# Optimization experiments

Hardware: AMD Instinct MI355X
Metric: run time of the kernel (lower is better)

## Reference

```python
import jax, jax.numpy as jnp
import numpy as np

D = 9  # nodefeat_n1 = 3 (resnet feat) + 6 (pos)


def _lstm_scan(x, Wih, Whh, bih, bhh, reverse=False):
    # x: [T, B, D] -> hidden states [T, B, D]; torch gate order i,f,g,o
    B = x.shape[1]
    def step(carry, xt):
        h, c = carry
        g = xt @ Wih.T + bih + h @ Whh.T + bhh
        i = jax.nn.sigmoid(g[:, :D])
        f = jax.nn.sigmoid(g[:, D:2*D])
        gg = jnp.tanh(g[:, 2*D:3*D])
        o = jax.nn.sigmoid(g[:, 3*D:])
        c = f * c + i * gg
        h = o * jnp.tanh(c)
        return (h, c), h
    init = (jnp.zeros((B, D), x.dtype), jnp.zeros((B, D), x.dtype))
    _, hs = jax.lax.scan(step, init, x, reverse=reverse)
    return hs


def _forward(nodes_feature, pos, attmat, msg_W, msg_b, gru_Wih, gru_Whh, gru_bih, gru_bhh,
             ro1_W, ro1_b, ro2_W, ro2_b, lf_Wih, lf_Whh, lf_bih, lf_bhh,
             lb_Wih, lb_Whh, lb_bih, lb_bhh, lr1_W, lr1_b, lr2_W, lr2_b, num_rec):
    node_feat = jnp.concatenate([nodes_feature, pos], axis=-1)  # [N,T,M,D]
    N, T, M, _ = node_feat.shape
    # valid_node_num = num_rec[b, 0] in the original code
    valid = (jnp.arange(M)[None, :] < num_rec[:, 0:1]).astype(node_feat.dtype)  # [N,M]
    att = attmat * valid[:, None, None, :]  # zero out invalid source nodes q
    src = node_feat  # message sources (h_w)
    hv = node_feat   # GRU hidden (h_v)
    hidden = node_feat
    for _ in range(2):  # iterN = 2 message-passing rounds
        msg = src @ msg_W.T + msg_b                    # [N,T,M,D] message_fc
        m = jnp.einsum('btnq,btqd->btnd', att, msg)    # attention-weighted sum over q
        # single-step GRU cell (torch gate order r,z,n)
        gx = m @ gru_Wih.T + gru_bih
        gh = hv @ gru_Whh.T + gru_bhh
        r = jax.nn.sigmoid(gx[..., :D] + gh[..., :D])
        z = jax.nn.sigmoid(gx[..., D:2*D] + gh[..., D:2*D])
        n = jnp.tanh(gx[..., 2*D:] + r * gh[..., 2*D:])
        h_new = (1.0 - z) * n + z * hv
        hidden = h_new * valid[:, None, :, None]       # invalid nodes never updated -> stay zero
        src = hidden
        hv = hidden
    vmask = valid[:, None, :, None]
    # per-frame readout (pred_label0)
    p0 = jax.nn.relu(hidden @ ro1_W.T + ro1_b) @ ro2_W.T + ro2_b
    pred_label0 = p0 * vmask
    # bidirectional LSTM over time, batched over (batch, node)
    x = hidden.transpose(1, 0, 2, 3).reshape(T, N * M, D)  # [T, N*M, D]
    hf = _lstm_scan(x, lf_Wih, lf_Whh, lf_bih, lf_bhh, reverse=False)
    hb = _lstm_scan(x, lb_Wih, lb_Whh, lb_bih, lb_bhh, reverse=True)
    out = jnp.concatenate([hf, hb], axis=-1).reshape(T, N, M, 2 * D).transpose(1, 0, 2, 3)
    p = jax.nn.relu(out @ lr1_W.T + lr1_b) @ lr2_W.T + lr2_b
    pred_label = p * vmask
    return pred_label, pred_label0


def setup_inputs() -> dict:
    key = jax.random.key(0)
    ks = jax.random.split(key, 32)
    N, T, M = 8192, 20, 6
    def u(k, shape, fan_in):
        s = 1.0 / np.sqrt(fan_in).astype(np.float32)
        return jax.random.uniform(k, shape, jnp.float32, -s, s)
    return {
        "nodes_feature": jax.random.normal(ks[0], (N, T, M, 3), jnp.float32),
        "pos": jax.random.normal(ks[1], (N, T, M, 6), jnp.float32),
        "attmat": jax.random.uniform(ks[2], (N, T, M, M), jnp.float32),
        "msg_W": u(ks[3], (D, D), D), "msg_b": u(ks[4], (D,), D),
        "gru_Wih": u(ks[5], (3 * D, D), D), "gru_Whh": u(ks[6], (3 * D, D), D),
        "gru_bih": u(ks[7], (3 * D,), D), "gru_bhh": u(ks[8], (3 * D,), D),
        "ro1_W": u(ks[9], (D, D), D), "ro1_b": u(ks[10], (D,), D),
        "ro2_W": u(ks[11], (7, D), D), "ro2_b": u(ks[12], (7,), D),
        "lf_Wih": u(ks[13], (4 * D, D), D), "lf_Whh": u(ks[14], (4 * D, D), D),
        "lf_bih": u(ks[15], (4 * D,), D), "lf_bhh": u(ks[16], (4 * D,), D),
        "lb_Wih": u(ks[17], (4 * D, D), D), "lb_Whh": u(ks[18], (4 * D, D), D),
        "lb_bih": u(ks[19], (4 * D,), D), "lb_bhh": u(ks[20], (4 * D,), D),
        "lr1_W": u(ks[21], (D, 2 * D), 2 * D), "lr1_b": u(ks[22], (D,), 2 * D),
        "lr2_W": u(ks[23], (7, D), D), "lr2_b": u(ks[24], (7,), D),
        "num_rec": jax.random.randint(ks[25], (N, T), 1, M + 1),
    }


def reference(nodes_feature, pos, attmat, msg_W, msg_b, gru_Wih, gru_Whh, gru_bih, gru_bhh,
              ro1_W, ro1_b, ro2_W, ro2_b, lf_Wih, lf_Whh, lf_bih, lf_bhh,
              lb_Wih, lb_Whh, lb_bih, lb_bhh, lr1_W, lr1_b, lr2_W, lr2_b, num_rec):
    return _forward(nodes_feature, pos, attmat, msg_W, msg_b, gru_Wih, gru_Whh, gru_bih, gru_bhh,
                    ro1_W, ro1_b, ro2_W, ro2_b, lf_Wih, lf_Whh, lf_bih, lf_bhh,
                    lb_Wih, lb_Whh, lb_bih, lb_bhh, lr1_W, lr1_b, lr2_W, lr2_b, num_rec)
```

## Files before the change

### kernel.cpp

```cpp
#include <hip/hip_runtime.h>

#define N_    8192
#define T_    20
#define M_    6
#define D_    9
#define NM_   (N_*M_)
#define NT_   (N_*T_)
#define NTM7_ (N_*T_*M_*7)

#define LOG2E 1.44269504088896f

typedef __attribute__((ext_vector_type(2))) float v2f;

__device__ __forceinline__ float sigm(float x){
    return __builtin_amdgcn_rcpf(1.f + __builtin_amdgcn_exp2f(-LOG2E * x));
}
__device__ __forceinline__ float tanh_(float x){
    return fmaf(2.f, __builtin_amdgcn_rcpf(1.f + __builtin_amdgcn_exp2f(-2.f*LOG2E * x)), -1.f);
}
__device__ __forceinline__ v2f splat(float s){ return (v2f){s, s}; }
__device__ __forceinline__ v2f sigm2(v2f x){ v2f r; r.x = sigm(x.x); r.y = sigm(x.y); return r; }
__device__ __forceinline__ v2f tanh2(v2f x){ v2f r; r.x = tanh_(x.x); r.y = tanh_(x.y); return r; }
__device__ __forceinline__ v2f relu2(v2f x){ v2f r; r.x = fmaxf(x.x,0.f); r.y = fmaxf(x.y,0.f); return r; }

__device__ __forceinline__ v2f pkfma(v2f a, v2f b, v2f acc){
    asm("v_pk_fma_f32 %0, %1, %2, %0" : "+v"(acc) : "v"(a), "v"(b));
    return acc;
}
__device__ __forceinline__ v2f pkmul(v2f a, v2f b){
    v2f d;
    asm("v_pk_mul_f32 %0, %1, %2" : "=v"(d) : "v"(a), "v"(b));
    return d;
}

__global__ __launch_bounds__(64) void k_fused(
    const float* __restrict__ nf,
    const float* __restrict__ pos,
    const float* __restrict__ am,
    const float* __restrict__ msgW, const float* __restrict__ msgb,
    const float* __restrict__ gWih, const float* __restrict__ gWhh,
    const float* __restrict__ gbih, const float* __restrict__ gbhh,
    const float* __restrict__ ro1W, const float* __restrict__ ro1b,
    const float* __restrict__ ro2W, const float* __restrict__ ro2b,
    const float* __restrict__ fWih, const float* __restrict__ fWhh,
    const float* __restrict__ fbih, const float* __restrict__ fbhh,
    const float* __restrict__ bWih, const float* __restrict__ bWhh,
    const float* __restrict__ bbih, const float* __restrict__ bbhh,
    const float* __restrict__ lr1W, const float* __restrict__ lr1b,
    const float* __restrict__ lr2W, const float* __restrict__ lr2b,
    const int*   __restrict__ numrec,
    float* __restrict__ out,
    float* __restrict__ out0)
{
    __shared__ float  hx[T_ * 3 * D_ * 2];
    __shared__ float4 hxs4[7 * 11];
    __shared__ v2f    shpool[640];

    const int lane = threadIdx.x & 63;
    const int n    = blockIdx.x;

    {
        const int g    = lane / 6;
        const int i    = lane - g * 6;
        const int gB   = g * 58;
        const bool lactive = (lane < 60);

        const int wbase = n * 20;
        const int ntA = lactive ? (wbase + g)      : wbase;
        const int ntB = lactive ? (wbase + 10 + g) : wbase;
        const int nA = ntA / T_, tA = ntA - nA * T_;
        const int nB = ntB / T_, tB = ntB - nB * T_;

        v2f s[D_];
        {
            const float* pA = nf + (size_t)ntA * 18 + i * 3;
            const float* pB = nf + (size_t)ntB * 18 + i * 3;
            #pragma unroll
            for (int k = 0; k < 3; ++k) { s[k].x = pA[k]; s[k].y = pB[k]; }
        }
        {
            const float2* pA = (const float2*)(pos + (size_t)ntA * 36 + i * 6);
            const float2* pB = (const float2*)(pos + (size_t)ntB * 36 + i * 6);
            #pragma unroll
            for (int k = 0; k < 3; ++k) {
                float2 a = pA[k], b = pB[k];
                s[3 + 2*k]     = (v2f){a.x, b.x};
                s[3 + 2*k + 1] = (v2f){a.y, b.y};
            }
        }
        v2f attr[M_];
        {
            const float2* pA = (const float2*)(am + (size_t)ntA * 36 + i * 6);
            const float2* pB = (const float2*)(am + (size_t)ntB * 36 + i * 6);
            #pragma unroll
            for (int k = 0; k < 3; ++k) {
                float2 a = pA[k], b = pB[k];
                attr[2*k]     = (v2f){a.x, b.x};
                attr[2*k + 1] = (v2f){a.y, b.y};
            }
        }
        const int nrA = numrec[nA * T_];
        const int nrB = numrec[nB * T_];
        #pragma unroll
        for (int q = 0; q < M_; ++q) {
            attr[q].x *= (q < nrA) ? 1.f : 0.f;
            attr[q].y *= (q < nrB) ? 1.f : 0.f;
        }
        v2f vmi; vmi.x = (i < nrA) ? 1.f : 0.f; vmi.y = (i < nrB) ? 1.f : 0.f;

        #pragma unroll
        for (int it = 0; it < 2; ++it) {
            #pragma unroll
            for (int d = 0; d < D_; ++d) {
                v2f a = splat(msgb[d]);
                #pragma unroll
                for (int k = 0; k < D_; ++k) a += s[k] * msgW[d*9 + k];
                shpool[gB + d*6 + i] = a;
            }
            v2f mm[D_];
            #pragma unroll
            for (int d = 0; d < D_; ++d) {
                const float4* rp = (const float4*)&shpool[gB + d*6];
                float4 p0 = rp[0], p1 = rp[1], p2 = rp[2];
                v2f a = pkmul(attr[0], (v2f){p0.x, p0.y});
                a = pkfma(attr[1], (v2f){p0.z, p0.w}, a);
                a = pkfma(attr[2], (v2f){p1.x, p1.y}, a);
                a = pkfma(attr[3], (v2f){p1.z, p1.w}, a);
                a = pkfma(attr[4], (v2f){p2.x, p2.y}, a);
                a = pkfma(attr[5], (v2f){p2.z, p2.w}, a);
                mm[d] = a;
            }
            v2f grz[18], gxn[9], ghn[9];
            #pragma unroll
            for (int j = 0; j < 18; ++j) {
                v2f a = splat(gbih[j] + gbhh[j]);
                #pragma unroll
                for (int k = 0; k < D_; ++k) {
                    a += mm[k] * gWih[j*9 + k];
                    a += s[k]  * gWhh[j*9 + k];
                }
                grz[j] = a;
            }
            #pragma unroll
            for (int j = 0; j < 9; ++j) {
                v2f ax = splat(gbih[18 + j]), ah = splat(gbhh[18 + j]);
                #pragma unroll
                for (int k = 0; k < D_; ++k) {
                    ax += mm[k] * gWih[(18 + j)*9 + k];
                    ah += s[k]  * gWhh[(18 + j)*9 + k];
                }
                gxn[j] = ax; ghn[j] = ah;
            }
            #pragma unroll
            for (int d = 0; d < D_; ++d) {
                v2f r  = sigm2(grz[d]);
                v2f z  = sigm2(grz[9 + d]);
                v2f nn = tanh2(gxn[d] + r * ghn[d]);
                s[d] = vmi * ((splat(1.f) - z) * nn + z * s[d]);
            }
        }

        if (lactive) {
            const int pr = i >> 1, par = i & 1;
            #pragma unroll
            for (int d = 0; d < D_; ++d) {
                hx[((tA*3 + pr)*9 + d)*2 + par] = s[d].x;
                hx[((tB*3 + pr)*9 + d)*2 + par] = s[d].y;
            }
        }

        v2f q9[D_];
        #pragma unroll
        for (int d = 0; d < D_; ++d) {
            v2f a = splat(ro1b[d]);
            #pragma unroll
            for (int k = 0; k < D_; ++k) a += s[k] * ro1W[d*9 + k];
            q9[d] = relu2(a);
        }
        if (lactive) {
            float* opA = out0 + (size_t)ntA * 42 + i * 7;
            float* opB = out0 + (size_t)ntB * 42 + i * 7;
            #pragma unroll
            for (int j = 0; j < 7; ++j) {
                v2f a = splat(ro2b[j]);
                #pragma unroll
                for (int k = 0; k < D_; ++k) a += q9[k] * ro2W[j*9 + k];
                a *= vmi;
                opA[j] = a.x; opB[j] = a.y;
            }
        }
    }

    __syncthreads();

    {
        int grpL = lane / 9;
        if (grpL == 7) grpL = 6;
        const int dd  = (lane == 63) ? 0 : (lane - grpL * 9);
        const bool sv   = (grpL < 6);
        const int  p    = sv ? (grpL % 3) : 0;
        const int  dir  = sv ? (grpL / 3) : 0;
        const int  xrow = grpL * 11;

        const float* Wih = dir ? bWih : fWih;
        const float* Whh = dir ? bWhh : fWhh;
        const float* Bih = dir ? bbih : fbih;
        const float* Bhh = dir ? bbhh : fbhh;

        float wxi[9], wxf[9], wxg[9], wxo[9];
        v2f   whi[9], whf[9], whg[9], who[9], w1r[9];
        #pragma unroll
        for (int k = 0; k < 9; ++k) {
            wxi[k] = Wih[(dd     )*9 + k];  whi[k] = splat(Whh[(dd     )*9 + k]);
            wxf[k] = Wih[(9  + dd)*9 + k];  whf[k] = splat(Whh[(9  + dd)*9 + k]);
            wxg[k] = Wih[(18 + dd)*9 + k];  whg[k] = splat(Whh[(18 + dd)*9 + k]);
            wxo[k] = Wih[(27 + dd)*9 + k];  who[k] = splat(Whh[(27 + dd)*9 + k]);
            w1r[k] = splat(lr1W[dd*18 + dir*9 + k]);
        }
        const float bi = Bih[dd]      + Bhh[dd];
        const float bf = Bih[9 + dd]  + Bhh[9 + dd];
        const float bg = Bih[18 + dd] + Bhh[18 + dd];
        const float bo = Bih[27 + dd] + Bhh[27 + dd];

        const int t0 = dir ? (T_ - 1) : 0;
        const int ts = dir ? -1 : 1;

        {
            v2f x0 = *(const v2f*)&hx[((t0*3 + p)*9 + dd)*2];
            hxs4[xrow + dd] = make_float4(0.f, 0.f, x0.x, x0.y);
        }
        v2f h = splat(0.f), c = splat(0.f);
        #pragma unroll 1
        for (int ss = 0; ss < T_; ++ss) {
            const int t = t0 + ts * ss;
            v2f xn = splat(0.f);
            if (ss < T_ - 1) xn = *(const v2f*)&hx[(((t + ts)*3 + p)*9 + dd)*2];

            v2f gi = splat(bi), gf = splat(bf), gg = splat(bg), go = splat(bo);
            v2f qc = splat(0.f);
            #pragma unroll
            for (int j = 0; j < 9; ++j) {
                float4 v = hxs4[xrow + j];
                v2f hj = (v2f){v.x, v.y}, xj = (v2f){v.z, v.w};
                gi = pkfma(hj, whi[j], gi);  gi += xj * wxi[j];
                gf = pkfma(hj, whf[j], gf);  gf += xj * wxf[j];
                gg = pkfma(hj, whg[j], gg);  gg += xj * wxg[j];
                go = pkfma(hj, who[j], go);  go += xj * wxo[j];
                qc = pkfma(hj, w1r[j], qc);
            }

            if (ss > 0 && sv) {
                const int tq = dir ? (20 - ss) : (ss - 1);
                const int qa = (p*20 + tq)*10 + dd;
                if (ss <= 10) shpool[qa] = qc;
                else          shpool[qa] += qc;
            }

            c = sigm2(gf) * c + sigm2(gi) * tanh2(gg);
            h = sigm2(go) * tanh2(c);
            hxs4[xrow + dd] = make_float4(h.x, h.y, xn.x, xn.y);
        }

        {
            v2f qc = splat(0.f);
            #pragma unroll
            for (int j = 0; j < 9; ++j) {
                float4 v = hxs4[xrow + j];
                qc = pkfma((v2f){v.x, v.y}, w1r[j], qc);
            }
            if (sv) {
                const int tq = dir ? 0 : 19;
                shpool[(p*20 + tq)*10 + dd] += qc;
            }
        }
    }

    __syncthreads();

    if (lane < 60) {
        const int pp = lane / 20;
        const int t  = lane - pp * 20;
        const v2f* qrow = &shpool[(pp*20 + t)*10];

        v2f q[9];
        #pragma unroll
        for (int dd2 = 0; dd2 < 9; ++dd2)
            q[dd2] = relu2(qrow[dd2] + splat(lr1b[dd2]));

        const int mA2 = 2 * pp, mB2 = mA2 + 1;
        const int nr = numrec[n * T_];
        v2f vi;
        vi.x = (mA2 < nr) ? 1.f : 0.f;
        vi.y = (mB2 < nr) ? 1.f : 0.f;

        float* opA = out + (size_t)((n * T_ + t) * M_ + mA2) * 7;
        float* opB = out + (size_t)((n * T_ + t) * M_ + mB2) * 7;
        #pragma unroll
        for (int j = 0; j < 7; ++j) {
            v2f a = splat(lr2b[j]);
            #pragma unroll
            for (int k = 0; k < 9; ++k) a += q[k] * lr2W[j*9 + k];
            a *= vi;
            opA[j] = a.x; opB[j] = a.y;
        }
    }
}

extern "C" void kernel_launch(void* const* d_in, const int* in_sizes, int n_in,
                              void* d_out, int out_size, void* d_ws, size_t ws_size,
                              hipStream_t stream) {
    const float* nf    = (const float*)d_in[0];
    const float* pos   = (const float*)d_in[1];
    const float* am    = (const float*)d_in[2];
    const float* msgW  = (const float*)d_in[3];
    const float* msgb  = (const float*)d_in[4];
    const float* gWih  = (const float*)d_in[5];
    const float* gWhh  = (const float*)d_in[6];
    const float* gbih  = (const float*)d_in[7];
    const float* gbhh  = (const float*)d_in[8];
    const float* ro1W  = (const float*)d_in[9];
    const float* ro1b  = (const float*)d_in[10];
    const float* ro2W  = (const float*)d_in[11];
    const float* ro2b  = (const float*)d_in[12];
    const float* lfWih = (const float*)d_in[13];
    const float* lfWhh = (const float*)d_in[14];
    const float* lfbih = (const float*)d_in[15];
    const float* lfbhh = (const float*)d_in[16];
    const float* lbWih = (const float*)d_in[17];
    const float* lbWhh = (const float*)d_in[18];
    const float* lbbih = (const float*)d_in[19];
    const float* lbbhh = (const float*)d_in[20];
    const float* lr1W  = (const float*)d_in[21];
    const float* lr1b  = (const float*)d_in[22];
    const float* lr2W  = (const float*)d_in[23];
    const float* lr2b  = (const float*)d_in[24];
    const int* numrec  = (const int*)d_in[25];

    float* outp = (float*)d_out;
    float* out0 = (float*)d_out + NTM7_;

    k_fused<<<N_, 64, 0, stream>>>(nf, pos, am, msgW, msgb, gWih, gWhh,
                                   gbih, gbhh, ro1W, ro1b, ro2W, ro2b,
                                   lfWih, lfWhh, lfbih, lfbhh,
                                   lbWih, lbWhh, lbbih, lbbhh,
                                   lr1W, lr1b, lr2W, lr2b, numrec,
                                   outp, out0);
}
```

Measured before the change: 266.4 us.

## Process two batch elements per block, interleaving their LSTM recurrences

```diff
diff --git a/kernel.cpp b/kernel.cpp
--- a/kernel.cpp
+++ b/kernel.cpp
@@ -52,14 +52,16 @@
     float* __restrict__ out,
     float* __restrict__ out0)
 {
-    __shared__ float  hx[T_ * 3 * D_ * 2];
-    __shared__ float4 hxs4[7 * 11];
-    __shared__ v2f    shpool[640];
+    __shared__ float  hx[2][T_ * 3 * D_ * 2];
+    __shared__ float4 hxs4[2][7 * 11];
+    __shared__ v2f    shpool[2][640];
 
     const int lane = threadIdx.x & 63;
-    const int n    = blockIdx.x;
-
-    {
+    const int n0   = blockIdx.x * 2;
+
+    #pragma unroll 1
+    for (int nn = 0; nn < 2; ++nn) {
+        const int n    = n0 + nn;
         const int g    = lane / 6;
         const int i    = lane - g * 6;
         const int gB   = g * 58;
@@ -115,12 +117,12 @@
                 v2f a = splat(msgb[d]);
                 #pragma unroll
                 for (int k = 0; k < D_; ++k) a += s[k] * msgW[d*9 + k];
-                shpool[gB + d*6 + i] = a;
+                shpool[nn][gB + d*6 + i] = a;
             }
             v2f mm[D_];
             #pragma unroll
             for (int d = 0; d < D_; ++d) {
-                const float4* rp = (const float4*)&shpool[gB + d*6];
+                const float4* rp = (const float4*)&shpool[nn][gB + d*6];
                 float4 p0 = rp[0], p1 = rp[1], p2 = rp[2];
                 v2f a = pkmul(attr[0], (v2f){p0.x, p0.y});
                 a = pkfma(attr[1], (v2f){p0.z, p0.w}, a);
@@ -155,8 +157,8 @@
             for (int d = 0; d < D_; ++d) {
                 v2f r  = sigm2(grz[d]);
                 v2f z  = sigm2(grz[9 + d]);
-                v2f nn = tanh2(gxn[d] + r * ghn[d]);
-                s[d] = vmi * ((splat(1.f) - z) * nn + z * s[d]);
+                v2f nn2 = tanh2(gxn[d] + r * ghn[d]);
+                s[d] = vmi * ((splat(1.f) - z) * nn2 + z * s[d]);
             }
         }
 
@@ -164,8 +166,8 @@
             const int pr = i >> 1, par = i & 1;
             #pragma unroll
             for (int d = 0; d < D_; ++d) {
-                hx[((tA*3 + pr)*9 + d)*2 + par] = s[d].x;
-                hx[((tB*3 + pr)*9 + d)*2 + par] = s[d].y;
+                hx[nn][((tA*3 + pr)*9 + d)*2 + par] = s[d].x;
+                hx[nn][((tB*3 + pr)*9 + d)*2 + par] = s[d].y;
             }
         }
 
@@ -224,84 +226,116 @@
 
         const int t0 = dir ? (T_ - 1) : 0;
         const int ts = dir ? -1 : 1;
-
-        {
-            v2f x0 = *(const v2f*)&hx[((t0*3 + p)*9 + dd)*2];
-            hxs4[xrow + dd] = make_float4(0.f, 0.f, x0.x, x0.y);
-        }
-        v2f h = splat(0.f), c = splat(0.f);
+        const int xoff = ((t0*3 + p)*9 + dd)*2;
+
+        {
+            v2f x0 = *(const v2f*)&hx[0][xoff];
+            hxs4[0][xrow + dd] = make_float4(0.f, 0.f, x0.x, x0.y);
+            v2f x1 = *(const v2f*)&hx[1][xoff];
+            hxs4[1][xrow + dd] = make_float4(0.f, 0.f, x1.x, x1.y);
+        }
+        v2f h0 = splat(0.f), c0 = splat(0.f);
+        v2f h1 = splat(0.f), c1 = splat(0.f);
+
         #pragma unroll 1
         for (int ss = 0; ss < T_; ++ss) {
             const int t = t0 + ts * ss;
-            v2f xn = splat(0.f);
-            if (ss < T_ - 1) xn = *(const v2f*)&hx[(((t + ts)*3 + p)*9 + dd)*2];
-
-            v2f gi = splat(bi), gf = splat(bf), gg = splat(bg), go = splat(bo);
-            v2f qc = splat(0.f);
+            v2f xn0 = splat(0.f), xn1 = splat(0.f);
+            if (ss < T_ - 1) {
+                const int xo = (((t + ts)*3 + p)*9 + dd)*2;
+                xn0 = *(const v2f*)&hx[0][xo];
+                xn1 = *(const v2f*)&hx[1][xo];
+            }
+
+            v2f gi0 = splat(bi), gf0 = splat(bf), gg0 = splat(bg), go0 = splat(bo);
+            v2f qc0 = splat(0.f);
             #pragma unroll
             for (int j = 0; j < 9; ++j) {
-                float4 v = hxs4[xrow + j];
+                float4 v = hxs4[0][xrow + j];
                 v2f hj = (v2f){v.x, v.y}, xj = (v2f){v.z, v.w};
-                gi = pkfma(hj, whi[j], gi);  gi += xj * wxi[j];
-                gf = pkfma(hj, whf[j], gf);  gf += xj * wxf[j];
-                gg = pkfma(hj, whg[j], gg);  gg += xj * wxg[j];
-                go = pkfma(hj, who[j], go);  go += xj * wxo[j];
-                qc = pkfma(hj, w1r[j], qc);
+                gi0 = pkfma(hj, whi[j], gi0);  gi0 += xj * wxi[j];
+                gf0 = pkfma(hj, whf[j], gf0);  gf0 += xj * wxf[j];
+                gg0 = pkfma(hj, whg[j], gg0);  gg0 += xj * wxg[j];
+                go0 = pkfma(hj, who[j], go0);  go0 += xj * wxo[j];
+                qc0 = pkfma(hj, w1r[j], qc0);
+            }
+            v2f gi1 = splat(bi), gf1 = splat(bf), gg1 = splat(bg), go1 = splat(bo);
+            v2f qc1 = splat(0.f);
+            #pragma unroll
+            for (int j = 0; j < 9; ++j) {
+                float4 v = hxs4[1][xrow + j];
+                v2f hj = (v2f){v.x, v.y}, xj = (v2f){v.z, v.w};
+                gi1 = pkfma(hj, whi[j], gi1);  gi1 += xj * wxi[j];
+                gf1 = pkfma(hj, whf[j], gf1);  gf1 += xj * wxf[j];
+                gg1 = pkfma(hj, whg[j], gg1);  gg1 += xj * wxg[j];
+                go1 = pkfma(hj, who[j], go1);  go1 += xj * wxo[j];
+                qc1 = pkfma(hj, w1r[j], qc1);
             }
 
             if (ss > 0 && sv) {
                 const int tq = dir ? (20 - ss) : (ss - 1);
                 const int qa = (p*20 + tq)*10 + dd;
-                if (ss <= 10) shpool[qa] = qc;
-                else          shpool[qa] += qc;
-            }
-
-            c = sigm2(gf) * c + sigm2(gi) * tanh2(gg);
-            h = sigm2(go) * tanh2(c);
-            hxs4[xrow + dd] = make_float4(h.x, h.y, xn.x, xn.y);
-        }
-
-        {
-            v2f qc = splat(0.f);
+                if (ss <= 10) { shpool[0][qa] = qc0;  shpool[1][qa] = qc1; }
+                else          { shpool[0][qa] += qc0; shpool[1][qa] += qc1; }
+            }
+
+            c0 = sigm2(gf0) * c0 + sigm2(gi0) * tanh2(gg0);
+            h0 = sigm2(go0) * tanh2(c0);
+            c1 = sigm2(gf1) * c1 + sigm2(gi1) * tanh2(gg1);
+            h1 = sigm2(go1) * tanh2(c1);
+
+            hxs4[0][xrow + dd] = make_float4(h0.x, h0.y, xn0.x, xn0.y);
+            hxs4[1][xrow + dd] = make_float4(h1.x, h1.y, xn1.x, xn1.y);
+        }
+
+        {
+            v2f qc0 = splat(0.f), qc1 = splat(0.f);
             #pragma unroll
             for (int j = 0; j < 9; ++j) {
-                float4 v = hxs4[xrow + j];
-                qc = pkfma((v2f){v.x, v.y}, w1r[j], qc);
+                float4 v0 = hxs4[0][xrow + j];
+                float4 v1 = hxs4[1][xrow + j];
+                qc0 = pkfma((v2f){v0.x, v0.y}, w1r[j], qc0);
+                qc1 = pkfma((v2f){v1.x, v1.y}, w1r[j], qc1);
             }
             if (sv) {
                 const int tq = dir ? 0 : 19;
-                shpool[(p*20 + tq)*10 + dd] += qc;
+                shpool[0][(p*20 + tq)*10 + dd] += qc0;
+                shpool[1][(p*20 + tq)*10 + dd] += qc1;
             }
         }
     }
 
     __syncthreads();
 
-    if (lane < 60) {
-        const int pp = lane / 20;
-        const int t  = lane - pp * 20;
-        const v2f* qrow = &shpool[(pp*20 + t)*10];
-
-        v2f q[9];
-        #pragma unroll
-        for (int dd2 = 0; dd2 < 9; ++dd2)
-            q[dd2] = relu2(qrow[dd2] + splat(lr1b[dd2]));
-
-        const int mA2 = 2 * pp, mB2 = mA2 + 1;
-        const int nr = numrec[n * T_];
-        v2f vi;
-        vi.x = (mA2 < nr) ? 1.f : 0.f;
-        vi.y = (mB2 < nr) ? 1.f : 0.f;
-
-        float* opA = out + (size_t)((n * T_ + t) * M_ + mA2) * 7;
-        float* opB = out + (size_t)((n * T_ + t) * M_ + mB2) * 7;
-        #pragma unroll
-        for (int j = 0; j < 7; ++j) {
-            v2f a = splat(lr2b[j]);
-            #pragma unroll
-            for (int k = 0; k < 9; ++k) a += q[k] * lr2W[j*9 + k];
-            a *= vi;
-            opA[j] = a.x; opB[j] = a.y;
+    #pragma unroll 1
+    for (int nn = 0; nn < 2; ++nn) {
+        if (lane < 60) {
+            const int n  = n0 + nn;
+            const int pp = lane / 20;
+            const int t  = lane - pp * 20;
+            const v2f* qrow = &shpool[nn][(pp*20 + t)*10];
+
+            v2f q[9];
+            #pragma unroll
+            for (int dd2 = 0; dd2 < 9; ++dd2)
+                q[dd2] = relu2(qrow[dd2] + splat(lr1b[dd2]));
+
+            const int mA2 = 2 * pp, mB2 = mA2 + 1;
+            const int nr = numrec[n * T_];
+            v2f vi;
+            vi.x = (mA2 < nr) ? 1.f : 0.f;
+            vi.y = (mB2 < nr) ? 1.f : 0.f;
+
+            float* opA = out + (size_t)((n * T_ + t) * M_ + mA2) * 7;
+            float* opB = out + (size_t)((n * T_ + t) * M_ + mB2) * 7;
+            #pragma unroll
+            for (int j = 0; j < 7; ++j) {
+                v2f a = splat(lr2b[j]);
+                #pragma unroll
+                for (int k = 0; k < 9; ++k) a += q[k] * lr2W[j*9 + k];
+                a *= vi;
+                opA[j] = a.x; opB[j] = a.y;
+            }
         }
     }
 }
@@ -339,10 +373,10 @@
     float* outp = (float*)d_out;
     float* out0 = (float*)d_out + NTM7_;
 
-    k_fused<<<N_, 64, 0, stream>>>(nf, pos, am, msgW, msgb, gWih, gWhh,
-                                   gbih, gbhh, ro1W, ro1b, ro2W, ro2b,
-                                   lfWih, lfWhh, lfbih, lfbhh,
-                                   lbWih, lbWhh, lbbih, lbbhh,
-                                   lr1W, lr1b, lr2W, lr2b, numrec,
-                                   outp, out0);
-}
+    k_fused<<<N_ / 2, 64, 0, stream>>>(nf, pos, am, msgW, msgb, gWih, gWhh,
+                                       gbih, gbhh, ro1W, ro1b, ro2W, ro2b,
+                                       lfWih, lfWhh, lfbih, lfbhh,
+                                       lbWih, lbWhh, lbbih, lbbhh,
+                                       lr1W, lr1b, lr2W, lr2b, numrec,
+                                       outp, out0);
+}
```

New measurement: 291.6 us. 9.5% more time.
